# Kernel optimization log

Hardware: AMD Instinct MI355X
Metric: run time of the kernel (lower is better)

## Reference

```python
import jax, jax.numpy as jnp
import numpy as np

B, L, H = 16, 4096, 512
D = 2 * H  # dim = hidden_dim * 2
SECL = 64


def setup_inputs() -> dict:
    key = jax.random.key(0)
    ks = jax.random.split(key, 10)
    return {
        "dec_hidden": jax.random.normal(ks[0], (B, D), jnp.float32),
        "enc_output": jax.random.normal(ks[1], (B, L, D), jnp.float32),
        "enc_feature": jax.random.normal(ks[2], (B, L, D), jnp.float32),
        "enc_mask": jax.random.uniform(ks[3], (B, L), jnp.float32),
        "sec_attn": jax.random.uniform(ks[4], (B, SECL), jnp.float32),
        "coverage": jax.random.uniform(ks[5], (B, L), jnp.float32),
        "W_feat": jax.random.normal(ks[6], (D, D), jnp.float32) * (1.0 / np.sqrt(D)),
        "b_feat": jax.random.normal(ks[7], (D,), jnp.float32) * 0.01,
        "w_score": jax.random.normal(ks[8], (D,), jnp.float32) * (1.0 / np.sqrt(D)),
        "w_cov": jax.random.normal(ks[9], (D,), jnp.float32) * 0.01,
    }


def reference(dec_hidden, enc_output, enc_feature, enc_mask, sec_attn, coverage,
              W_feat, b_feat, w_score, w_cov):
    # dec_feature = feat(dec_hidden), broadcast over src_len (repeat in torch)
    dec_feature = dec_hidden @ W_feat.T + b_feat            # [B, D]
    att = enc_feature + dec_feature[:, None, :]             # [B, L, D]
    # coverage feature: feat_cov(coverage.view(-1,1)) -> outer product with w_cov
    att = att + coverage[..., None] * w_cov                 # [B, L, D]
    score = jnp.einsum('bld,d->bl', jnp.tanh(att), w_score)  # score_v, [B, L]
    # NOTE: the original computes einsum('bl,bl->bl', sec_attn_expanded, score)
    # but immediately overwrites it -> dead code; sec_attn does not affect output.
    attn = jax.nn.softmax(score, axis=1) * enc_mask         # masked softmax
    attn = attn / attn.sum(axis=1, keepdims=True)           # utils.normalize
    context = jnp.einsum('bl,bld->bd', attn, enc_output)    # bmm -> [B, D]
    new_coverage = attn + coverage                          # use_coverage branch
    return attn, context, new_coverage
```

## Files before the change

kernel.cpp:

```cpp
#include <hip/hip_runtime.h>
#include <math.h>

#define NB 16
#define NL 4096
#define ND 1024
#define CHUNKS 64
#define ROWS_PER_CHUNK (NL / CHUNKS)

__device__ __forceinline__ float fast_tanh(float x) {
    float e = __expf(2.0f * x);
    return 1.0f - 2.0f / (e + 1.0f);
}

__global__ __launch_bounds__(256) void k_dec_feature(
    const float* __restrict__ dec_hidden,
    const float* __restrict__ W_feat,
    const float* __restrict__ b_feat,
    float* __restrict__ dec_feature)
{
    int gw   = blockIdx.x * 4 + (threadIdx.x >> 6);
    int lane = threadIdx.x & 63;
    int d = gw >> 4;
    int b = gw & 15;
    const float4* wrow = (const float4*)(W_feat + (size_t)d * ND);
    const float4* hrow = (const float4*)(dec_hidden + (size_t)b * ND);
    float acc = 0.f;
#pragma unroll
    for (int i = 0; i < 4; ++i) {
        float4 w = wrow[i * 64 + lane];
        float4 h = hrow[i * 64 + lane];
        acc += w.x * h.x + w.y * h.y + w.z * h.z + w.w * h.w;
    }
#pragma unroll
    for (int off = 32; off > 0; off >>= 1)
        acc += __shfl_down(acc, off);
    if (lane == 0)
        dec_feature[b * ND + d] = acc + b_feat[d];
}

__global__ __launch_bounds__(256) void k_score(
    const float* __restrict__ enc_feature,
    const float* __restrict__ dec_feature,
    const float* __restrict__ coverage,
    const float* __restrict__ w_cov,
    const float* __restrict__ w_score,
    float* __restrict__ score)
{
    int gw   = blockIdx.x * 4 + (threadIdx.x >> 6);
    int lane = threadIdx.x & 63;
    int b = gw >> 12;
    const float4* erow = (const float4*)(enc_feature + (size_t)gw * ND);
    const float4* frow = (const float4*)(dec_feature + (size_t)b * ND);
    const float4* wc   = (const float4*)w_cov;
    const float4* wsc  = (const float4*)w_score;
    float cov = coverage[gw];
    float acc = 0.f;
#pragma unroll
    for (int i = 0; i < 4; ++i) {
        float4 e = erow[i * 64 + lane];
        float4 f = frow[i * 64 + lane];
        float4 c = wc [i * 64 + lane];
        float4 s = wsc[i * 64 + lane];
        acc += fast_tanh(e.x + f.x + cov * c.x) * s.x;
        acc += fast_tanh(e.y + f.y + cov * c.y) * s.y;
        acc += fast_tanh(e.z + f.z + cov * c.z) * s.z;
        acc += fast_tanh(e.w + f.w + cov * c.w) * s.w;
    }
#pragma unroll
    for (int off = 32; off > 0; off >>= 1)
        acc += __shfl_down(acc, off);
    if (lane == 0)
        score[gw] = acc;
}

__global__ __launch_bounds__(256) void k_softmax(
    const float* __restrict__ score,
    const float* __restrict__ enc_mask,
    const float* __restrict__ coverage,
    float* __restrict__ attn,
    float* __restrict__ new_cov)
{
    __shared__ float s_em[NL];
    __shared__ float s_red[4];
    __shared__ float s_sum[4];
    int b = blockIdx.x;
    int t = threadIdx.x;
    const float* srow = score    + (size_t)b * NL;
    const float* mrow = enc_mask + (size_t)b * NL;
    const float* crow = coverage + (size_t)b * NL;

    float m = -INFINITY;
    for (int i = t; i < NL; i += 256) m = fmaxf(m, srow[i]);
#pragma unroll
    for (int off = 32; off > 0; off >>= 1) m = fmaxf(m, __shfl_xor(m, off));
    if ((t & 63) == 0) s_red[t >> 6] = m;
    __syncthreads();
    float bm = fmaxf(fmaxf(s_red[0], s_red[1]), fmaxf(s_red[2], s_red[3]));

    float sum = 0.f;
    for (int i = t; i < NL; i += 256) {
        float em = __expf(srow[i] - bm) * mrow[i];
        s_em[i] = em;
        sum += em;
    }
#pragma unroll
    for (int off = 32; off > 0; off >>= 1) sum += __shfl_xor(sum, off);
    if ((t & 63) == 0) s_sum[t >> 6] = sum;
    __syncthreads();
    float inv = 1.0f / (s_sum[0] + s_sum[1] + s_sum[2] + s_sum[3]);

    for (int i = t; i < NL; i += 256) {
        float a = s_em[i] * inv;
        attn   [(size_t)b * NL + i] = a;
        new_cov[(size_t)b * NL + i] = a + crow[i];
    }
}

__global__ __launch_bounds__(256) void k_context_partial(
    const float* __restrict__ enc_output,
    const float* __restrict__ attn,
    float* __restrict__ partial)
{
    int bc = blockIdx.x;
    int b  = bc >> 6;
    int c  = bc & 63;
    int t  = threadIdx.x;
    int l0 = c * ROWS_PER_CHUNK;
    const float4* base = (const float4*)(enc_output + ((size_t)(b * NL + l0)) * ND);
    const float*  arow = attn + (size_t)b * NL + l0;
    float4 acc = make_float4(0.f, 0.f, 0.f, 0.f);
#pragma unroll 4
    for (int r = 0; r < ROWS_PER_CHUNK; ++r) {
        float  a = arow[r];
        float4 e = base[(size_t)r * 256 + t];
        acc.x += a * e.x; acc.y += a * e.y; acc.z += a * e.z; acc.w += a * e.w;
    }
    ((float4*)(partial + (size_t)bc * ND))[t] = acc;
}

__global__ __launch_bounds__(256) void k_context_reduce(
    const float* __restrict__ partial,
    float* __restrict__ context)
{
    int blk = blockIdx.x;
    int b = blk >> 2;
    int d = (blk & 3) * 256 + threadIdx.x;
    const float* p = partial + (size_t)b * CHUNKS * ND + d;
    float acc = 0.f;
#pragma unroll 8
    for (int c = 0; c < CHUNKS; ++c) acc += p[(size_t)c * ND];
    context[(size_t)b * ND + d] = acc;
}

extern "C" void kernel_launch(void* const* d_in, const int* in_sizes, int n_in,
                              void* d_out, int out_size, void* d_ws, size_t ws_size,
                              hipStream_t stream) {
    const float* dec_hidden  = (const float*)d_in[0];
    const float* enc_output  = (const float*)d_in[1];
    const float* enc_feature = (const float*)d_in[2];
    const float* enc_mask    = (const float*)d_in[3];
    const float* coverage    = (const float*)d_in[5];
    const float* W_feat      = (const float*)d_in[6];
    const float* b_feat      = (const float*)d_in[7];
    const float* w_score     = (const float*)d_in[8];
    const float* w_cov       = (const float*)d_in[9];

    float* out      = (float*)d_out;
    float* attn_out = out;
    float* ctx_out  = out + NB * NL;
    float* cov_out  = out + NB * NL + NB * ND;

    float* ws          = (float*)d_ws;
    float* dec_feature = ws;
    float* score       = ws + NB * ND;
    float* partial     = ws + NB * ND + NB * NL;

    k_dec_feature<<<dim3((NB * ND) / 4), dim3(256), 0, stream>>>(
        dec_hidden, W_feat, b_feat, dec_feature);

    k_score<<<dim3((NB * NL) / 4), dim3(256), 0, stream>>>(
        enc_feature, dec_feature, coverage, w_cov, w_score, score);

    k_softmax<<<dim3(NB), dim3(256), 0, stream>>>(
        score, enc_mask, coverage, attn_out, cov_out);

    k_context_partial<<<dim3(NB * CHUNKS), dim3(256), 0, stream>>>(
        enc_output, attn_out, partial);

    k_context_reduce<<<dim3((NB * ND) / 256), dim3(256), 0, stream>>>(
        partial, ctx_out);
}
```

Baseline: 532.8 us.

## Split softmax into parallel stats, fuse normalization into context, batch score rows

The single-block-per-batch softmax is replaced by a parallel partial max/sum kernel and a tiny combine kernel. Attention normalization, attn/coverage output writes and the context partial product now run in one fused kernel. The score kernel processes four rows per wave, reusing the register-held dec_feature and weight vectors. Nontemporal loads are used for the large streaming tensors. This adds an extra kernel launch and recomputes exp per chunk, and the masked partial sums must combine correctly.

```diff
diff --git a/kernel.cpp b/kernel.cpp
--- a/kernel.cpp
+++ b/kernel.cpp
@@ -10,6 +10,13 @@
 __device__ __forceinline__ float fast_tanh(float x) {
     float e = __expf(2.0f * x);
     return 1.0f - 2.0f / (e + 1.0f);
+}
+
+typedef float nativef4 __attribute__((ext_vector_type(4)));
+
+__device__ __forceinline__ float4 nt_load4(const float4* p) {
+    nativef4 v = __builtin_nontemporal_load((const nativef4*)p);
+    return make_float4(v.x, v.y, v.z, v.w);
 }
 
 __global__ __launch_bounds__(256) void k_dec_feature(
@@ -46,93 +53,125 @@
     const float* __restrict__ w_score,
     float* __restrict__ score)
 {
-    int gw   = blockIdx.x * 4 + (threadIdx.x >> 6);
+    int wid  = blockIdx.x * 4 + (threadIdx.x >> 6);
     int lane = threadIdx.x & 63;
-    int b = gw >> 12;
-    const float4* erow = (const float4*)(enc_feature + (size_t)gw * ND);
+    int r0 = wid * 4;
+    int b  = r0 >> 12;
+
     const float4* frow = (const float4*)(dec_feature + (size_t)b * ND);
     const float4* wc   = (const float4*)w_cov;
     const float4* wsc  = (const float4*)w_score;
-    float cov = coverage[gw];
-    float acc = 0.f;
+    float4 f4[4], c4[4], s4[4];
 #pragma unroll
     for (int i = 0; i < 4; ++i) {
-        float4 e = erow[i * 64 + lane];
-        float4 f = frow[i * 64 + lane];
-        float4 c = wc [i * 64 + lane];
-        float4 s = wsc[i * 64 + lane];
-        acc += fast_tanh(e.x + f.x + cov * c.x) * s.x;
-        acc += fast_tanh(e.y + f.y + cov * c.y) * s.y;
-        acc += fast_tanh(e.z + f.z + cov * c.z) * s.z;
-        acc += fast_tanh(e.w + f.w + cov * c.w) * s.w;
-    }
+        f4[i] = frow[i * 64 + lane];
+        c4[i] = wc  [i * 64 + lane];
+        s4[i] = wsc [i * 64 + lane];
+    }
+
+#pragma unroll
+    for (int r = 0; r < 4; ++r) {
+        int row = r0 + r;
+        float cov = coverage[row];
+        const float4* erow = (const float4*)(enc_feature + (size_t)row * ND);
+        float acc = 0.f;
+#pragma unroll
+        for (int i = 0; i < 4; ++i) {
+            float4 e = nt_load4(&erow[i * 64 + lane]);
+            acc += fast_tanh(e.x + f4[i].x + cov * c4[i].x) * s4[i].x;
+            acc += fast_tanh(e.y + f4[i].y + cov * c4[i].y) * s4[i].y;
+            acc += fast_tanh(e.z + f4[i].z + cov * c4[i].z) * s4[i].z;
+            acc += fast_tanh(e.w + f4[i].w + cov * c4[i].w) * s4[i].w;
+        }
+#pragma unroll
+        for (int off = 32; off > 0; off >>= 1)
+            acc += __shfl_down(acc, off);
+        if (lane == 0)
+            score[row] = acc;
+    }
+}
+
+__global__ __launch_bounds__(256) void k_stats(
+    const float* __restrict__ score,
+    const float* __restrict__ enc_mask,
+    float* __restrict__ pmax,
+    float* __restrict__ psum)
+{
+    int w    = blockIdx.x * 4 + (threadIdx.x >> 6);
+    int lane = threadIdx.x & 63;
+    int b = w >> 4, j = w & 15;
+    const float4* s4 = (const float4*)(score    + (size_t)b * NL + j * 256);
+    const float4* m4 = (const float4*)(enc_mask + (size_t)b * NL + j * 256);
+    float4 s  = s4[lane];
+    float4 mk = m4[lane];
+    float mx = fmaxf(fmaxf(s.x, s.y), fmaxf(s.z, s.w));
 #pragma unroll
     for (int off = 32; off > 0; off >>= 1)
-        acc += __shfl_down(acc, off);
-    if (lane == 0)
-        score[gw] = acc;
-}
-
-__global__ __launch_bounds__(256) void k_softmax(
+        mx = fmaxf(mx, __shfl_xor(mx, off));
+    float es = __expf(s.x - mx) * mk.x + __expf(s.y - mx) * mk.y
+             + __expf(s.z - mx) * mk.z + __expf(s.w - mx) * mk.w;
+#pragma unroll
+    for (int off = 32; off > 0; off >>= 1)
+        es += __shfl_xor(es, off);
+    if (lane == 0) { pmax[w] = mx; psum[w] = es; }
+}
+
+__global__ __launch_bounds__(256) void k_combine(
+    const float* __restrict__ pmax,
+    const float* __restrict__ psum,
+    float* __restrict__ Mb,
+    float* __restrict__ invb)
+{
+    int t = threadIdx.x;
+    int b = t >> 4, j = t & 15;
+    float m = pmax[b * 16 + j];
+    float s = psum[b * 16 + j];
+    float M = m;
+#pragma unroll
+    for (int off = 8; off > 0; off >>= 1)
+        M = fmaxf(M, __shfl_xor(M, off, 16));
+    float sc = s * __expf(m - M);
+#pragma unroll
+    for (int off = 8; off > 0; off >>= 1)
+        sc += __shfl_xor(sc, off, 16);
+    if (j == 0) { Mb[b] = M; invb[b] = 1.0f / sc; }
+}
+
+__global__ __launch_bounds__(256) void k_context_attn(
+    const float* __restrict__ enc_output,
     const float* __restrict__ score,
     const float* __restrict__ enc_mask,
     const float* __restrict__ coverage,
-    float* __restrict__ attn,
-    float* __restrict__ new_cov)
-{
-    __shared__ float s_em[NL];
-    __shared__ float s_red[4];
-    __shared__ float s_sum[4];
-    int b = blockIdx.x;
-    int t = threadIdx.x;
-    const float* srow = score    + (size_t)b * NL;
-    const float* mrow = enc_mask + (size_t)b * NL;
-    const float* crow = coverage + (size_t)b * NL;
-
-    float m = -INFINITY;
-    for (int i = t; i < NL; i += 256) m = fmaxf(m, srow[i]);
-#pragma unroll
-    for (int off = 32; off > 0; off >>= 1) m = fmaxf(m, __shfl_xor(m, off));
-    if ((t & 63) == 0) s_red[t >> 6] = m;
-    __syncthreads();
-    float bm = fmaxf(fmaxf(s_red[0], s_red[1]), fmaxf(s_red[2], s_red[3]));
-
-    float sum = 0.f;
-    for (int i = t; i < NL; i += 256) {
-        float em = __expf(srow[i] - bm) * mrow[i];
-        s_em[i] = em;
-        sum += em;
-    }
-#pragma unroll
-    for (int off = 32; off > 0; off >>= 1) sum += __shfl_xor(sum, off);
-    if ((t & 63) == 0) s_sum[t >> 6] = sum;
-    __syncthreads();
-    float inv = 1.0f / (s_sum[0] + s_sum[1] + s_sum[2] + s_sum[3]);
-
-    for (int i = t; i < NL; i += 256) {
-        float a = s_em[i] * inv;
-        attn   [(size_t)b * NL + i] = a;
-        new_cov[(size_t)b * NL + i] = a + crow[i];
-    }
-}
-
-__global__ __launch_bounds__(256) void k_context_partial(
-    const float* __restrict__ enc_output,
-    const float* __restrict__ attn,
+    const float* __restrict__ Mb,
+    const float* __restrict__ invb,
+    float* __restrict__ attn_out,
+    float* __restrict__ cov_out,
     float* __restrict__ partial)
 {
+    __shared__ float s_a[ROWS_PER_CHUNK];
     int bc = blockIdx.x;
     int b  = bc >> 6;
     int c  = bc & 63;
     int t  = threadIdx.x;
     int l0 = c * ROWS_PER_CHUNK;
+
+    float M   = Mb[b];
+    float inv = invb[b];
+    if (t < ROWS_PER_CHUNK) {
+        size_t l = (size_t)b * NL + l0 + t;
+        float a = __expf(score[l] - M) * enc_mask[l] * inv;
+        s_a[t] = a;
+        attn_out[l] = a;
+        cov_out [l] = a + coverage[l];
+    }
+    __syncthreads();
+
     const float4* base = (const float4*)(enc_output + ((size_t)(b * NL + l0)) * ND);
-    const float*  arow = attn + (size_t)b * NL + l0;
     float4 acc = make_float4(0.f, 0.f, 0.f, 0.f);
 #pragma unroll 4
     for (int r = 0; r < ROWS_PER_CHUNK; ++r) {
-        float  a = arow[r];
-        float4 e = base[(size_t)r * 256 + t];
+        float  a = s_a[r];
+        float4 e = nt_load4(&base[(size_t)r * 256 + t]);
         acc.x += a * e.x; acc.y += a * e.y; acc.z += a * e.z; acc.w += a * e.w;
     }
     ((float4*)(partial + (size_t)bc * ND))[t] = acc;
@@ -172,20 +211,26 @@
 
     float* ws          = (float*)d_ws;
     float* dec_feature = ws;
-    float* score       = ws + NB * ND;
-    float* partial     = ws + NB * ND + NB * NL;
+    float* score       = dec_feature + NB * ND;
+    float* partial     = score + NB * NL;
+    float* pmax        = partial + NB * CHUNKS * ND;
+    float* psum        = pmax + 256;
+    float* Mb          = psum + 256;
+    float* invb        = Mb + 16;
 
     k_dec_feature<<<dim3((NB * ND) / 4), dim3(256), 0, stream>>>(
         dec_hidden, W_feat, b_feat, dec_feature);
 
-    k_score<<<dim3((NB * NL) / 4), dim3(256), 0, stream>>>(
+    k_score<<<dim3((NB * NL) / 16), dim3(256), 0, stream>>>(
         enc_feature, dec_feature, coverage, w_cov, w_score, score);
 
-    k_softmax<<<dim3(NB), dim3(256), 0, stream>>>(
-        score, enc_mask, coverage, attn_out, cov_out);
-
-    k_context_partial<<<dim3(NB * CHUNKS), dim3(256), 0, stream>>>(
-        enc_output, attn_out, partial);
+    k_stats<<<dim3(64), dim3(256), 0, stream>>>(score, enc_mask, pmax, psum);
+
+    k_combine<<<dim3(1), dim3(256), 0, stream>>>(pmax, psum, Mb, invb);
+
+    k_context_attn<<<dim3(NB * CHUNKS), dim3(256), 0, stream>>>(
+        enc_output, score, enc_mask, coverage, Mb, invb,
+        attn_out, cov_out, partial);
 
     k_context_reduce<<<dim3((NB * ND) / 256), dim3(256), 0, stream>>>(
         partial, ctx_out);
```

New measurement: 513.5 us. -3.6%, faster.
